# Kernel optimization log

Hardware: AMD Instinct MI355X
Metric: run time of the kernel (lower is better)

## Reference

```python
import jax, jax.numpy as jnp
import numpy as np

SXY_BF, SC_BF = 70.0, 12.0
COMPAT_BF, COMPAT_SPATIAL = 4.0, 2.0
SXY_SPATIAL = 6
NUM_ITER = 5
N_OUT = 21


def _gkern_depthwise(std, chans):
    # matches gkern(): sig_sq even -> r = sig_sq - 1, s = 2r+1
    sig_sq = std ** 2
    r = sig_sq if sig_sq % 2 else sig_sq - 1
    s = 2 * r + 1
    yy, xx = np.meshgrid(np.arange(s), np.arange(s), indexing='ij')
    k = np.exp(-(((yy - r) ** 2 + (xx - r) ** 2) / (2.0 * sig_sq)))
    k = k / k.sum()
    # original builds a [C,C,s,s] diagonal kernel == depthwise [C,1,s,s]
    return jnp.asarray(np.broadcast_to(k[None, None], (chans, 1, s, s)).copy(), jnp.float32)


def setup_inputs() -> dict:
    key = jax.random.key(0)
    k1, k2 = jax.random.split(key)
    unary = jax.random.uniform(k1, (2, N_OUT, 64, 64), dtype=jnp.float32)
    ref = jax.random.uniform(k2, (2, 3, 64, 64), dtype=jnp.float32) * 255.0  # RGB image
    gk = _gkern_depthwise(SXY_SPATIAL, N_OUT)
    kstd = jnp.asarray([SXY_BF, SXY_BF, SC_BF, SC_BF, SC_BF], jnp.float32)
    return {"unary": unary, "ref": ref, "gk": gk, "kstd": kstd}


def _crf_forward(unary, ref, gk, kstd):
    N, C, H, W = unary.shape
    P = H * W
    # stacked reference features: [y, x, r, g, b]
    yy, xx = jnp.meshgrid(jnp.arange(H, dtype=jnp.float32),
                          jnp.arange(W, dtype=jnp.float32), indexing='ij')
    grid = jnp.broadcast_to(jnp.stack([yy, xx])[None], (N, 2, H, W))
    stacked = jnp.concatenate([grid, ref], axis=1)  # [N,5,H,W]
    feats = (stacked / kstd[None, :, None, None]).reshape(N, -1, P).transpose(0, 2, 1)  # [N,P,5]
    # exact dense Gaussian (bilateral) kernel: K[p,q] = exp(-||f_p - f_q||^2 / 2)
    sq = jnp.sum(feats * feats, axis=-1)  # [N,P]
    d2 = sq[:, :, None] + sq[:, None, :] - 2.0 * jnp.einsum('npd,nqd->npq', feats, feats)
    K = jnp.exp(-0.5 * jnp.maximum(d2, 0.0))  # [N,P,P]

    U = jnp.log(jnp.clip(unary, 1e-5, 1.0))
    q = jax.nn.softmax(U, axis=1)
    pad = gk.shape[-1] // 2
    for i in range(NUM_ITER):
        qbf = jnp.einsum('npq,ncq->ncp', K, q.reshape(N, C, P)).reshape(N, C, H, W)
        qsf = jax.lax.conv_general_dilated(
            q, gk, window_strides=(1, 1), padding=[(pad, pad), (pad, pad)],
            feature_group_count=C, dimension_numbers=('NCHW', 'OIHW', 'NCHW'))
        q_hat = U + COMPAT_BF * qbf + COMPAT_SPATIAL * qsf
        q = jax.nn.softmax(q_hat, axis=1)  # normalize_final_iter=True
    return q


def reference(unary, ref, gk, kstd):
    return _crf_forward(unary, ref, gk, kstd)
```

## Files before the change

### kernel.cpp

```cpp
#include <hip/hip_runtime.h>
#include <math.h>

#ifndef __has_builtin
#define __has_builtin(x) 0
#endif
#if __has_builtin(__builtin_amdgcn_exp2f)
#define EXP2F(x) __builtin_amdgcn_exp2f(x)
#else
#define EXP2F(x) exp2f(x)
#endif

#define L2E  1.44269504088896340736f
#define RL2E 0.69314718055994530942f

#define NBATCH 2
#define NC 21
#define NP 4096
#define KR 35
#define KS 71

typedef _Float16 half_t;
typedef _Float16 h8 __attribute__((ext_vector_type(8)));
typedef _Float16 h4 __attribute__((ext_vector_type(4)));
typedef float f4 __attribute__((ext_vector_type(4)));
typedef float f2 __attribute__((ext_vector_type(2)));
#define MFMA16(a, b, c) __builtin_amdgcn_mfma_f32_16x16x32_f16((a), (b), (c), 0, 0, 0)

static __device__ __forceinline__ f2 pk_fma(f2 a, f2 b, f2 c) {
    f2 d;
    asm volatile("v_pk_fma_f32 %0, %1, %2, %3" : "=v"(d) : "v"(a), "v"(b), "v"(c));
    return d;
}
static __device__ __forceinline__ f2 pk_add(f2 a, f2 b) {
    f2 d;
    asm volatile("v_pk_add_f32 %0, %1, %2" : "=v"(d) : "v"(a), "v"(b));
    return d;
}

#define PTILE 128
#define NPT   32
#define SQ    16
#define CHUNK 256
#define STEPS 8
#define NBBIL (NBATCH * NPT * SQ)
#define NBCONV (NBATCH * NC)
#define SEGS_PER_S 1024
#define SEG_HALVES 256

#define OFF_QFEAT 0
#define OFF_QSOA  65536
#define OFF_UT    114688
#define OFF_QSF   311296
#define OFF_G     483328
#define OFF_QH16  485376
#define OFF_PART  845824

#define LDS_BYTES 27648
#define QLS_STRIDE 264

__global__ __launch_bounds__(256) void setup_kernel(
    const float* __restrict__ unary, const float* __restrict__ ref,
    const float* __restrict__ kstd, float* __restrict__ ws,
    float* __restrict__ outq)
{
    int gid = blockIdx.x * 256 + threadIdx.x;
    if (gid < 4096) {
        float s = 0.f;
        for (int t = -KR; t <= KR; ++t) s += expf(-(float)(t * t) * (1.0f / 72.0f));
        int y = gid >> 6, yp = gid & 63;
        int d = y - yp;
        float v = (d >= -KR && d <= KR) ? expf(-(float)(d * d) * (1.0f / 72.0f)) / s : 0.f;
        ((half_t*)(ws + OFF_G))[gid] = (half_t)v;
    }
    if (gid >= NBATCH * NP) return;
    int n = gid >> 12, p = gid & (NP - 1);
    int y = p >> 6, x = p & 63;
    float k0 = kstd[0], k1 = kstd[1], k2 = kstd[2], k3 = kstd[3], k4 = kstd[4];
    const float* rp = ref + n * 3 * NP + p;
    float f0 = (float)y / k0;
    float f1 = (float)x / k1;
    float f2_ = rp[0]      / k2;
    float f3 = rp[NP]     / k3;
    float f4_ = rp[2 * NP] / k4;
    float sq = f0*f0 + f1*f1 + f2_*f2_ + f3*f3 + f4_*f4_;
    float h  = -0.5f * L2E * sq;
    float* qf = ws + OFF_QFEAT + gid * 8;
    qf[0]=L2E*f0; qf[1]=L2E*f1; qf[2]=L2E*f2_; qf[3]=L2E*f3; qf[4]=L2E*f4_;
    qf[5]=h; qf[6]=0.f; qf[7]=0.f;
    float* qs = ws + OFF_QSOA;
    qs[0*8192 + gid] = L2E*f0;  qs[1*8192 + gid] = L2E*f1;
    qs[2*8192 + gid] = L2E*f2_; qs[3*8192 + gid] = L2E*f3;
    qs[4*8192 + gid] = L2E*f4_; qs[5*8192 + gid] = h;

    float U[NC], e[NC];
    const float* up = unary + n * NC * NP + p;
    float m = -1e30f;
    for (int c = 0; c < NC; ++c) {
        float u = up[c * NP];
        u = fminf(fmaxf(u, 1e-5f), 1.0f);
        U[c] = logf(u);
        m = fmaxf(m, U[c]);
    }
    float ssum = 0.f;
    for (int c = 0; c < NC; ++c) { e[c] = EXP2F(L2E * (U[c] - m)); ssum += e[c]; }
    float inv = 1.0f / ssum;
    float* ut = ws + OFF_UT + gid * 24;
    half_t* qh = (half_t*)(ws + OFF_QH16);
    for (int c = 0; c < NC; ++c) {
        float qv = e[c] * inv;
        ut[c] = U[c];
        qh[(n * 24 + c) * NP + p] = (half_t)qv;
        outq[(n * NC + c) * NP + p] = qv;
    }
    ut[21] = 0.f; ut[22] = 0.f; ut[23] = 0.f;
    qh[(n * 24 + 21) * NP + p] = (half_t)0.f;
    qh[(n * 24 + 22) * NP + p] = (half_t)0.f;
    qh[(n * 24 + 23) * NP + p] = (half_t)0.f;
}

__global__ __launch_bounds__(256) void bilat_conv_kernel(
    const float* __restrict__ qfeatA,
    const float* __restrict__ qsoa,
    const half_t* __restrict__ qh16,
    const half_t* __restrict__ gmat,
    half_t* __restrict__ part,
    float* __restrict__ qsf)
{
    __shared__ __align__(16) char lds[LDS_BYTES];
    int b = blockIdx.x;
    int tid = threadIdx.x;
    int l = tid & 63, w = tid >> 6;

    if (b < NBBIL) {
        int n  = b & 1;
        int pt = (b >> 1) & (NPT - 1);
        int s  = b >> 6;
        float*  qsoaS = (float*)lds;
        half_t* qls   = (half_t*)(lds + 6144);

        for (int i = tid; i < 6 * (CHUNK / 4); i += 256) {
            int d = i >> 6, g = i & 63;
            *(f4*)(qsoaS + d * CHUNK + g * 4) =
                *(const f4*)(qsoa + (size_t)d * 8192 + n * NP + s * CHUNK + g * 4);
        }
        for (int i = tid; i < 21 * (CHUNK / 8); i += 256) {
            int c = i >> 5, g = i & 31;
            *(h8*)(qls + c * QLS_STRIDE + g * 8) =
                *(const h8*)(qh16 + (size_t)(n * 24 + c) * NP + s * CHUNK + g * 8);
        }
        for (int i = tid; i < 11 * 33; i += 256) {
            int c = 21 + i / 33, g = i % 33;
            *(h8*)(qls + c * QLS_STRIDE + g * 8) = (h8)(half_t)0.f;
        }
        f2 pf2[2][5], ph2[2];
        #pragma unroll
        for (int mt = 0; mt < 2; ++mt) {
            const float* fp = qfeatA + (size_t)(n * NP + pt * PTILE + (w * 2 + mt) * 16 + (l & 15)) * 8;
            #pragma unroll
            for (int i = 0; i < 5; ++i) {
                float v = fp[i] * RL2E;
                pf2[mt][i] = (f2){v, v};
            }
            ph2[mt] = (f2){fp[5], fp[5]};
        }
        f4 acc[2][2];
        #pragma unroll
        for (int mt = 0; mt < 2; ++mt) { acc[mt][0] = (f4)0.f; acc[mt][1] = (f4)0.f; }
        int kq = (l >> 4) * 8;
        __syncthreads();

        for (int step = 0; step < STEPS; ++step) {
            int qbase = step * 32 + kq;
            h8 kv[2];
            #pragma unroll
            for (int hf = 0; hf < 2; ++hf) {
                f4 qf0 = *(const f4*)(qsoaS + 0 * CHUNK + qbase + hf * 4);
                f4 qf1 = *(const f4*)(qsoaS + 1 * CHUNK + qbase + hf * 4);
                f4 qf2 = *(const f4*)(qsoaS + 2 * CHUNK + qbase + hf * 4);
                f4 qf3 = *(const f4*)(qsoaS + 3 * CHUNK + qbase + hf * 4);
                f4 qf4 = *(const f4*)(qsoaS + 4 * CHUNK + qbase + hf * 4);
                f4 qf5 = *(const f4*)(qsoaS + 5 * CHUNK + qbase + hf * 4);
                #pragma unroll
                for (int pr = 0; pr < 2; ++pr) {
                    f2 q0 = {qf0[2*pr], qf0[2*pr+1]};
                    f2 q1 = {qf1[2*pr], qf1[2*pr+1]};
                    f2 q2 = {qf2[2*pr], qf2[2*pr+1]};
                    f2 q3 = {qf3[2*pr], qf3[2*pr+1]};
                    f2 q4 = {qf4[2*pr], qf4[2*pr+1]};
                    f2 qh2 = {qf5[2*pr], qf5[2*pr+1]};
                    #pragma unroll
                    for (int mt = 0; mt < 2; ++mt) {
                        f2 e = pk_add(qh2, ph2[mt]);
                        e = pk_fma(pf2[mt][0], q0, e);
                        e = pk_fma(pf2[mt][1], q1, e);
                        e = pk_fma(pf2[mt][2], q2, e);
                        e = pk_fma(pf2[mt][3], q3, e);
                        e = pk_fma(pf2[mt][4], q4, e);
                        kv[mt][hf * 4 + pr * 2]     = (half_t)EXP2F(e[0]);
                        kv[mt][hf * 4 + pr * 2 + 1] = (half_t)EXP2F(e[1]);
                    }
                }
            }
            h8 bf0 = *(const h8*)(qls + (size_t)(l & 15) * QLS_STRIDE + qbase);
            h8 bf1 = *(const h8*)(qls + (size_t)(16 + (l & 15)) * QLS_STRIDE + qbase);
            #pragma unroll
            for (int mt = 0; mt < 2; ++mt) {
                acc[mt][0] = MFMA16(kv[mt], bf0, acc[mt][0]);
                acc[mt][1] = MFMA16(kv[mt], bf1, acc[mt][1]);
            }
        }
        #pragma unroll
        for (int mt = 0; mt < 2; ++mt) {
            #pragma unroll
            for (int cht = 0; cht < 2; ++cht) {
                int segFlat = ((((s * 2 + n) * NPT + pt) * 4 + w) * 2 + mt) * 2 + cht;
                h4 hv;
                hv[0] = (half_t)acc[mt][cht][0];
                hv[1] = (half_t)acc[mt][cht][1];
                hv[2] = (half_t)acc[mt][cht][2];
                hv[3] = (half_t)acc[mt][cht][3];
                *(h4*)(part + (size_t)segFlat * SEG_HALVES + l * 4) = hv;
            }
        }
    } else {
        int cb = b - NBBIL;
        int n = cb / NC, c = cb % NC;
        half_t* qt = (half_t*)lds;
        half_t* gl = (half_t*)(lds + 9216);
        half_t* dl = (half_t*)(lds + 18432);

        for (int i = tid; i < 512; i += 256) {
            int row = i >> 3, g = i & 7;
            *(h8*)(gl + row * 72 + g * 8) = *(const h8*)(gmat + row * 64 + g * 8);
        }
        const half_t* qsrc = qh16 + (size_t)(n * 24 + c) * NP;
        for (int i = tid; i < 512; i += 256) {
            int row = i >> 3, g = i & 7;
            h8 v = *(const h8*)(qsrc + row * 64 + g * 8);
            #pragma unroll
            for (int k = 0; k < 8; ++k) qt[(g * 8 + k) * 72 + row] = v[k];
        }
        __syncthreads();

        int m0 = w * 16;
        f4 acc1[4];
        #pragma unroll
        for (int nt = 0; nt < 4; ++nt) acc1[nt] = (f4)0.f;
        #pragma unroll
        for (int ks = 0; ks < 2; ++ks) {
            h8 af = *(const h8*)(gl + (size_t)(m0 + (l & 15)) * 72 + ks * 32 + (l >> 4) * 8);
            #pragma unroll
            for (int nt = 0; nt < 4; ++nt) {
                h8 bf = *(const h8*)(qt + (size_t)(nt * 16 + (l & 15)) * 72 + ks * 32 + (l >> 4) * 8);
                acc1[nt] = MFMA16(af, bf, acc1[nt]);
            }
        }
        #pragma unroll
        for (int nt = 0; nt < 4; ++nt)
            #pragma unroll
            for (int r = 0; r < 4; ++r)
                dl[(size_t)(m0 + (l >> 4) * 4 + r) * 72 + nt * 16 + (l & 15)] = (half_t)acc1[nt][r];
        __syncthreads();

        f4 acc2[4];
        #pragma unroll
        for (int nt = 0; nt < 4; ++nt) acc2[nt] = (f4)0.f;
        #pragma unroll
        for (int ks = 0; ks < 2; ++ks) {
            h8 af = *(const h8*)(dl + (size_t)(m0 + (l & 15)) * 72 + ks * 32 + (l >> 4) * 8);
            #pragma unroll
            for (int nt = 0; nt < 4; ++nt) {
                h8 bf = *(const h8*)(gl + (size_t)(nt * 16 + (l & 15)) * 72 + ks * 32 + (l >> 4) * 8);
                acc2[nt] = MFMA16(af, bf, acc2[nt]);
            }
        }
        float* dst = qsf + (size_t)(n * NC + c) * NP;
        #pragma unroll
        for (int nt = 0; nt < 4; ++nt)
            #pragma unroll
            for (int r = 0; r < 4; ++r)
                dst[(size_t)(m0 + (l >> 4) * 4 + r) * 64 + nt * 16 + (l & 15)] = acc2[nt][r];
    }
}

__global__ __launch_bounds__(256) void reduce_update_kernel(
    const half_t* __restrict__ part, const float* __restrict__ ut_,
    const float* __restrict__ qsf, float* __restrict__ outq,
    half_t* __restrict__ qh16)
{
    __shared__ float red[4096];
    int rb = blockIdx.x;
    int tid = threadIdx.x;
    int n = rb & 1, pt = rb >> 1;

    float acc[16];
    #pragma unroll
    for (int k = 0; k < 16; ++k) acc[k] = 0.f;
    for (int s = 0; s < SQ; ++s) {
        size_t base = (size_t)(((s * 2 + n) * NPT + pt) * 16) * SEG_HALVES;
        #pragma unroll
        for (int k = 0; k < 4; ++k) {
            h4 v = *(const h4*)(part + base + (size_t)(k * 256 + tid) * 4);
            acc[k*4+0] += (float)v[0]; acc[k*4+1] += (float)v[1];
            acc[k*4+2] += (float)v[2]; acc[k*4+3] += (float)v[3];
        }
    }
    #pragma unroll
    for (int k = 0; k < 4; ++k)
        *(f4*)(red + (k * 256 + tid) * 4) =
            (f4){acc[k*4+0], acc[k*4+1], acc[k*4+2], acc[k*4+3]};
    __syncthreads();

    if (tid < PTILE) {
        int pp = tid;
        int p = pt * PTILE + pp;
        int gid = n * NP + p;
        int mt_g = pp >> 4;
        int wv = mt_g >> 1, mtl = mt_g & 1;
        int mrow = pp & 15;
        int lg = mrow >> 2, reg = mrow & 3;
        int segL = wv * 4 + mtl * 2;

        float lg_[NC], e[NC];
        const float* ut = ut_ + (size_t)gid * 24;
        const float* qs = qsf + (size_t)n * NC * NP + p;
        float m = -1e30f;
        #pragma unroll
        for (int c = 0; c < NC; ++c) {
            int cht = c >> 4, chL = c & 15;
            float qb = red[(segL + cht) * 256 + (lg * 16 + chL) * 4 + reg];
            float li = ut[c] + 4.0f * qb + 2.0f * qs[c * NP];
            lg_[c] = li;
            m = fmaxf(m, li);
        }
        float ssum = 0.f;
        #pragma unroll
        for (int c = 0; c < NC; ++c) { e[c] = EXP2F(L2E * (lg_[c] - m)); ssum += e[c]; }
        float inv = 1.0f / ssum;
        #pragma unroll
        for (int c = 0; c < NC; ++c) {
            float qv = e[c] * inv;
            outq[(size_t)(n * NC + c) * NP + p] = qv;
            qh16[(size_t)(n * 24 + c) * NP + p] = (half_t)qv;
        }
    }
}

extern "C" void kernel_launch(void* const* d_in, const int* in_sizes, int n_in,
                              void* d_out, int out_size, void* d_ws, size_t ws_size,
                              hipStream_t stream)
{
    const float* unary = (const float*)d_in[0];
    const float* ref   = (const float*)d_in[1];
    const float* kstd  = (const float*)d_in[3];
    float* ws   = (float*)d_ws;
    float* outq = (float*)d_out;

    const float*  qfeatA = ws + OFF_QFEAT;
    const float*  qsoa   = ws + OFF_QSOA;
    float*        ut     = ws + OFF_UT;
    float*        qsf    = ws + OFF_QSF;
    const half_t* gmat   = (const half_t*)(ws + OFF_G);
    half_t*       qh16   = (half_t*)(ws + OFF_QH16);
    half_t*       part   = (half_t*)(ws + OFF_PART);

    setup_kernel<<<32, 256, 0, stream>>>(unary, ref, kstd, ws, outq);
    for (int it = 0; it < 5; ++it) {
        bilat_conv_kernel<<<NBBIL + NBCONV, 256, 0, stream>>>(
            qfeatA, qsoa, qh16, gmat, part, qsf);
        reduce_update_kernel<<<64, 256, 0, stream>>>(part, ut, qsf, outq, qh16);
    }
}
```

Baseline: 155.0 us.

## Fuse setup and all CRF iterations into one cooperative persistent kernel

Replaces the eleven separate launches (setup, then bilateral/conv and reduce/update per iteration) with a single cooperative kernel. It uses grid-wide syncs between phases and keeps the query-feature chunk in LDS across iterations. Per-launch overhead and pipeline drain between tiny kernels should go away. The costs are the grid.sync barriers, a grid capped at 1024 co-resident blocks, and conv blocks doubling as bilateral blocks, which serialises work that used to run on extra blocks. The old multi-kernel path remains as a fallback when cooperative launch is unavailable.

```diff
diff --git a/kernel.cpp b/kernel.cpp
--- a/kernel.cpp
+++ b/kernel.cpp
@@ -1,5 +1,8 @@
 #include <hip/hip_runtime.h>
+#include <hip/hip_cooperative_groups.h>
 #include <math.h>
+
+namespace cg = cooperative_groups;
 
 #ifndef __has_builtin
 #define __has_builtin(x) 0
@@ -17,7 +20,7 @@
 #define NC 21
 #define NP 4096
 #define KR 35
-#define KS 71
+#define NUM_ITER 5
 
 typedef _Float16 half_t;
 typedef _Float16 h8 __attribute__((ext_vector_type(8)));
@@ -44,7 +47,6 @@
 #define STEPS 8
 #define NBBIL (NBATCH * NPT * SQ)
 #define NBCONV (NBATCH * NC)
-#define SEGS_PER_S 1024
 #define SEG_HALVES 256
 
 #define OFF_QFEAT 0
@@ -55,8 +57,293 @@
 #define OFF_QH16  485376
 #define OFF_PART  845824
 
-#define LDS_BYTES 27648
 #define QLS_STRIDE 264
+
+__global__ __launch_bounds__(256, 4) void crf_fused(
+    const float* __restrict__ unary, const float* __restrict__ ref,
+    const float* __restrict__ kstd, float* __restrict__ ws,
+    float* __restrict__ outq)
+{
+    __shared__ __align__(16) char lds[33792];
+    cg::grid_group grid = cg::this_grid();
+    const int b = blockIdx.x;
+    const int tid = threadIdx.x;
+    const int l = tid & 63, w = tid >> 6;
+
+    float*  qfeatA = ws + OFF_QFEAT;
+    float*  qsoa   = ws + OFF_QSOA;
+    float*  utb    = ws + OFF_UT;
+    float*  qsf    = ws + OFF_QSF;
+    half_t* gmat   = (half_t*)(ws + OFF_G);
+    half_t* qh16   = (half_t*)(ws + OFF_QH16);
+    half_t* part   = (half_t*)(ws + OFF_PART);
+
+    {
+        int gid = b * 256 + tid;
+        if (gid < 4096) {
+            float gs = 0.f;
+            for (int t = -KR; t <= KR; ++t) gs += expf(-(float)(t * t) * (1.0f / 72.0f));
+            int y = gid >> 6, yp = gid & 63;
+            int d = y - yp;
+            float v = (d >= -KR && d <= KR) ? expf(-(float)(d * d) * (1.0f / 72.0f)) / gs : 0.f;
+            gmat[gid] = (half_t)v;
+        }
+        if (gid < NBATCH * NP) {
+            int n = gid >> 12, p = gid & (NP - 1);
+            int y = p >> 6, x = p & 63;
+            float k0 = kstd[0], k1 = kstd[1], k2 = kstd[2], k3 = kstd[3], k4 = kstd[4];
+            const float* rp = ref + n * 3 * NP + p;
+            float f0 = (float)y / k0;
+            float f1 = (float)x / k1;
+            float f2_ = rp[0]      / k2;
+            float f3 = rp[NP]     / k3;
+            float f4_ = rp[2 * NP] / k4;
+            float sq = f0*f0 + f1*f1 + f2_*f2_ + f3*f3 + f4_*f4_;
+            float h  = -0.5f * L2E * sq;
+            float* qf = qfeatA + gid * 8;
+            qf[0]=L2E*f0; qf[1]=L2E*f1; qf[2]=L2E*f2_; qf[3]=L2E*f3; qf[4]=L2E*f4_;
+            qf[5]=h; qf[6]=0.f; qf[7]=0.f;
+            qsoa[0*8192 + gid] = L2E*f0;  qsoa[1*8192 + gid] = L2E*f1;
+            qsoa[2*8192 + gid] = L2E*f2_; qsoa[3*8192 + gid] = L2E*f3;
+            qsoa[4*8192 + gid] = L2E*f4_; qsoa[5*8192 + gid] = h;
+
+            float U[NC], eU[NC];
+            const float* up = unary + n * NC * NP + p;
+            float m = -1e30f;
+            for (int c = 0; c < NC; ++c) {
+                float u = up[c * NP];
+                u = fminf(fmaxf(u, 1e-5f), 1.0f);
+                U[c] = logf(u);
+                m = fmaxf(m, U[c]);
+            }
+            float ssum = 0.f;
+            for (int c = 0; c < NC; ++c) { eU[c] = EXP2F(L2E * (U[c] - m)); ssum += eU[c]; }
+            float inv = 1.0f / ssum;
+            float* utp = utb + gid * 24;
+            for (int c = 0; c < NC; ++c) {
+                utp[c] = U[c];
+                qh16[(n * 24 + c) * NP + p] = (half_t)(eU[c] * inv);
+            }
+            utp[21] = 0.f; utp[22] = 0.f; utp[23] = 0.f;
+            qh16[(n * 24 + 21) * NP + p] = (half_t)0.f;
+            qh16[(n * 24 + 22) * NP + p] = (half_t)0.f;
+            qh16[(n * 24 + 23) * NP + p] = (half_t)0.f;
+        }
+    }
+    grid.sync();
+
+    const int nB  = b & 1;
+    const int ptB = (b >> 1) & (NPT - 1);
+    const int sB  = b >> 6;
+
+    {
+        float* qsoaS = (float*)lds;
+        for (int i = tid; i < 6 * (CHUNK / 4); i += 256) {
+            int d = i >> 6, g = i & 63;
+            *(f4*)(qsoaS + d * CHUNK + g * 4) =
+                *(const f4*)(qsoa + (size_t)d * 8192 + nB * NP + sB * CHUNK + g * 4);
+        }
+    }
+
+    for (int it = 0; it < NUM_ITER; ++it) {
+        {
+            float*  qsoaS = (float*)lds;
+            half_t* qls   = (half_t*)(lds + 6144);
+
+            for (int i = tid; i < 21 * (CHUNK / 8); i += 256) {
+                int c = i >> 5, g = i & 31;
+                *(h8*)(qls + c * QLS_STRIDE + g * 8) =
+                    *(const h8*)(qh16 + (size_t)(nB * 24 + c) * NP + sB * CHUNK + g * 8);
+            }
+            if (it == 0 || b < NBCONV) {
+                for (int i = tid; i < 11 * 33; i += 256) {
+                    int c = 21 + i / 33, g = i % 33;
+                    *(h8*)(qls + c * QLS_STRIDE + g * 8) = (h8)(half_t)0.f;
+                }
+            }
+            f2 pf2[2][5], ph2[2];
+            #pragma unroll
+            for (int mt = 0; mt < 2; ++mt) {
+                const float* fp = qfeatA + (size_t)(nB * NP + ptB * PTILE + (w * 2 + mt) * 16 + (l & 15)) * 8;
+                #pragma unroll
+                for (int i = 0; i < 5; ++i) {
+                    float v = fp[i] * RL2E;
+                    pf2[mt][i] = (f2){v, v};
+                }
+                ph2[mt] = (f2){fp[5], fp[5]};
+            }
+            f4 acc[2][2];
+            #pragma unroll
+            for (int mt = 0; mt < 2; ++mt) { acc[mt][0] = (f4)0.f; acc[mt][1] = (f4)0.f; }
+            int kq = (l >> 4) * 8;
+            __syncthreads();
+
+            for (int step = 0; step < STEPS; ++step) {
+                int qbase = step * 32 + kq;
+                h8 kv[2];
+                #pragma unroll
+                for (int hf = 0; hf < 2; ++hf) {
+                    f4 qf0 = *(const f4*)(qsoaS + 0 * CHUNK + qbase + hf * 4);
+                    f4 qf1 = *(const f4*)(qsoaS + 1 * CHUNK + qbase + hf * 4);
+                    f4 qf2 = *(const f4*)(qsoaS + 2 * CHUNK + qbase + hf * 4);
+                    f4 qf3 = *(const f4*)(qsoaS + 3 * CHUNK + qbase + hf * 4);
+                    f4 qf4 = *(const f4*)(qsoaS + 4 * CHUNK + qbase + hf * 4);
+                    f4 qf5 = *(const f4*)(qsoaS + 5 * CHUNK + qbase + hf * 4);
+                    #pragma unroll
+                    for (int pr = 0; pr < 2; ++pr) {
+                        f2 q0 = {qf0[2*pr], qf0[2*pr+1]};
+                        f2 q1 = {qf1[2*pr], qf1[2*pr+1]};
+                        f2 q2 = {qf2[2*pr], qf2[2*pr+1]};
+                        f2 q3 = {qf3[2*pr], qf3[2*pr+1]};
+                        f2 q4 = {qf4[2*pr], qf4[2*pr+1]};
+                        f2 qh2 = {qf5[2*pr], qf5[2*pr+1]};
+                        #pragma unroll
+                        for (int mt = 0; mt < 2; ++mt) {
+                            f2 e = pk_add(qh2, ph2[mt]);
+                            e = pk_fma(pf2[mt][0], q0, e);
+                            e = pk_fma(pf2[mt][1], q1, e);
+                            e = pk_fma(pf2[mt][2], q2, e);
+                            e = pk_fma(pf2[mt][3], q3, e);
+                            e = pk_fma(pf2[mt][4], q4, e);
+                            kv[mt][hf * 4 + pr * 2]     = (half_t)EXP2F(e[0]);
+                            kv[mt][hf * 4 + pr * 2 + 1] = (half_t)EXP2F(e[1]);
+                        }
+                    }
+                }
+                h8 bf0 = *(const h8*)(qls + (size_t)(l & 15) * QLS_STRIDE + qbase);
+                h8 bf1 = *(const h8*)(qls + (size_t)(16 + (l & 15)) * QLS_STRIDE + qbase);
+                #pragma unroll
+                for (int mt = 0; mt < 2; ++mt) {
+                    acc[mt][0] = MFMA16(kv[mt], bf0, acc[mt][0]);
+                    acc[mt][1] = MFMA16(kv[mt], bf1, acc[mt][1]);
+                }
+            }
+            #pragma unroll
+            for (int mt = 0; mt < 2; ++mt) {
+                #pragma unroll
+                for (int cht = 0; cht < 2; ++cht) {
+                    int segFlat = ((((sB * 2 + nB) * NPT + ptB) * 4 + w) * 2 + mt) * 2 + cht;
+                    h4 hv;
+                    hv[0] = (half_t)acc[mt][cht][0];
+                    hv[1] = (half_t)acc[mt][cht][1];
+                    hv[2] = (half_t)acc[mt][cht][2];
+                    hv[3] = (half_t)acc[mt][cht][3];
+                    *(h4*)(part + (size_t)segFlat * SEG_HALVES + l * 4) = hv;
+                }
+            }
+        }
+
+        if (b < NBCONV) {
+            __syncthreads();
+            int n2 = b / NC, c2 = b % NC;
+            half_t* qt = (half_t*)(lds + 6144);
+            half_t* gl = (half_t*)(lds + 15360);
+            half_t* dl = (half_t*)(lds + 24576);
+
+            for (int i = tid; i < 512; i += 256) {
+                int row = i >> 3, g = i & 7;
+                *(h8*)(gl + row * 72 + g * 8) = *(const h8*)(gmat + row * 64 + g * 8);
+            }
+            const half_t* qsrc = qh16 + (size_t)(n2 * 24 + c2) * NP;
+            for (int i = tid; i < 512; i += 256) {
+                int row = i >> 3, g = i & 7;
+                h8 v = *(const h8*)(qsrc + row * 64 + g * 8);
+                #pragma unroll
+                for (int k = 0; k < 8; ++k) qt[(g * 8 + k) * 72 + row] = v[k];
+            }
+            __syncthreads();
+
+            int m0 = w * 16;
+            f4 acc1[4];
+            #pragma unroll
+            for (int nt = 0; nt < 4; ++nt) acc1[nt] = (f4)0.f;
+            #pragma unroll
+            for (int ks = 0; ks < 2; ++ks) {
+                h8 af = *(const h8*)(gl + (size_t)(m0 + (l & 15)) * 72 + ks * 32 + (l >> 4) * 8);
+                #pragma unroll
+                for (int nt = 0; nt < 4; ++nt) {
+                    h8 bf = *(const h8*)(qt + (size_t)(nt * 16 + (l & 15)) * 72 + ks * 32 + (l >> 4) * 8);
+                    acc1[nt] = MFMA16(af, bf, acc1[nt]);
+                }
+            }
+            #pragma unroll
+            for (int nt = 0; nt < 4; ++nt)
+                #pragma unroll
+                for (int r = 0; r < 4; ++r)
+                    dl[(size_t)(m0 + (l >> 4) * 4 + r) * 72 + nt * 16 + (l & 15)] = (half_t)acc1[nt][r];
+            __syncthreads();
+
+            f4 acc2[4];
+            #pragma unroll
+            for (int nt = 0; nt < 4; ++nt) acc2[nt] = (f4)0.f;
+            #pragma unroll
+            for (int ks = 0; ks < 2; ++ks) {
+                h8 af = *(const h8*)(dl + (size_t)(m0 + (l & 15)) * 72 + ks * 32 + (l >> 4) * 8);
+                #pragma unroll
+                for (int nt = 0; nt < 4; ++nt) {
+                    h8 bf = *(const h8*)(gl + (size_t)(nt * 16 + (l & 15)) * 72 + ks * 32 + (l >> 4) * 8);
+                    acc2[nt] = MFMA16(af, bf, acc2[nt]);
+                }
+            }
+            float* dst = qsf + (size_t)(n2 * NC + c2) * NP;
+            #pragma unroll
+            for (int nt = 0; nt < 4; ++nt)
+                #pragma unroll
+                for (int r = 0; r < 4; ++r)
+                    dst[(size_t)(m0 + (l >> 4) * 4 + r) * 64 + nt * 16 + (l & 15)] = acc2[nt][r];
+        }
+        grid.sync();
+
+        if (b < 256) {
+            int n = b & 1, pt = (b >> 1) & 31, wq = b >> 6;
+            float* red = (float*)(lds + 6144);
+            int lseg = w;
+            float a0 = 0.f, a1 = 0.f, a2 = 0.f, a3 = 0.f;
+            for (int s = 0; s < SQ; ++s) {
+                size_t segF = (size_t)((((s * 2 + n) * NPT + pt) * 4 + wq) * 4 + lseg);
+                h4 v = *(const h4*)(part + segF * SEG_HALVES + (size_t)l * 4);
+                a0 += (float)v[0]; a1 += (float)v[1]; a2 += (float)v[2]; a3 += (float)v[3];
+            }
+            *(f4*)(red + tid * 4) = (f4){a0, a1, a2, a3};
+            __syncthreads();
+
+            if (tid < 32) {
+                int pp = tid;
+                int p = pt * PTILE + wq * 32 + pp;
+                int gid = n * NP + p;
+                int mtl = pp >> 4, mrow = pp & 15;
+                int lg2 = mrow >> 2, reg = mrow & 3;
+
+                const float* ut = utb + (size_t)gid * 24;
+                const float* qs = qsf + (size_t)n * NC * NP + p;
+                float e[NC];
+                float m = -1e30f;
+                #pragma unroll
+                for (int c = 0; c < NC; ++c) {
+                    int cht = c >> 4, chL = c & 15;
+                    float qb = red[(mtl * 2 + cht) * 256 + (lg2 * 16 + chL) * 4 + reg];
+                    float li = ut[c] + 4.0f * qb + 2.0f * qs[c * NP];
+                    e[c] = li;
+                    m = fmaxf(m, li);
+                }
+                float ssum = 0.f;
+                #pragma unroll
+                for (int c = 0; c < NC; ++c) { float v = EXP2F(L2E * (e[c] - m)); e[c] = v; ssum += v; }
+                float inv = 1.0f / ssum;
+                if (it == NUM_ITER - 1) {
+                    #pragma unroll
+                    for (int c = 0; c < NC; ++c)
+                        outq[(size_t)(n * NC + c) * NP + p] = e[c] * inv;
+                } else {
+                    #pragma unroll
+                    for (int c = 0; c < NC; ++c)
+                        qh16[(size_t)(n * 24 + c) * NP + p] = (half_t)(e[c] * inv);
+                }
+            }
+        }
+        if (it < NUM_ITER - 1) grid.sync();
+    }
+}
 
 __global__ __launch_bounds__(256) void setup_kernel(
     const float* __restrict__ unary, const float* __restrict__ ref,
@@ -119,14 +406,11 @@
 }
 
 __global__ __launch_bounds__(256) void bilat_conv_kernel(
-    const float* __restrict__ qfeatA,
-    const float* __restrict__ qsoa,
-    const half_t* __restrict__ qh16,
-    const half_t* __restrict__ gmat,
-    half_t* __restrict__ part,
-    float* __restrict__ qsf)
+    const float* __restrict__ qfeatA, const float* __restrict__ qsoa,
+    const half_t* __restrict__ qh16, const half_t* __restrict__ gmat,
+    half_t* __restrict__ part, float* __restrict__ qsf)
 {
-    __shared__ __align__(16) char lds[LDS_BYTES];
+    __shared__ __align__(16) char lds[27648];
     int b = blockIdx.x;
     int tid = threadIdx.x;
     int l = tid & 63, w = tid >> 6;
@@ -356,18 +640,38 @@
     float* ws   = (float*)d_ws;
     float* outq = (float*)d_out;
 
-    const float*  qfeatA = ws + OFF_QFEAT;
-    const float*  qsoa   = ws + OFF_QSOA;
-    float*        ut     = ws + OFF_UT;
-    float*        qsf    = ws + OFF_QSF;
-    const half_t* gmat   = (const half_t*)(ws + OFF_G);
-    half_t*       qh16   = (half_t*)(ws + OFF_QH16);
-    half_t*       part   = (half_t*)(ws + OFF_PART);
-
-    setup_kernel<<<32, 256, 0, stream>>>(unary, ref, kstd, ws, outq);
-    for (int it = 0; it < 5; ++it) {
-        bilat_conv_kernel<<<NBBIL + NBCONV, 256, 0, stream>>>(
-            qfeatA, qsoa, qh16, gmat, part, qsf);
-        reduce_update_kernel<<<64, 256, 0, stream>>>(part, ut, qsf, outq, qh16);
+    static int coop_ok = -1;
+    if (coop_ok < 0) {
+        int dev = 0, has = 0, nb = 0, ncu = 0;
+        (void)hipGetDevice(&dev);
+        (void)hipDeviceGetAttribute(&has, hipDeviceAttributeCooperativeLaunch, dev);
+        (void)hipDeviceGetAttribute(&ncu, hipDeviceAttributeMultiprocessorCount, dev);
+        (void)hipOccupancyMaxActiveBlocksPerMultiprocessor(&nb, crf_fused, 256, 0);
+        coop_ok = (has && (long)nb * ncu >= NBBIL) ? 1 : 0;
+    }
+
+    int launched = 0;
+    if (coop_ok) {
+        void* kargs[] = {(void*)&unary, (void*)&ref, (void*)&kstd, (void*)&ws, (void*)&outq};
+        hipError_t err = hipLaunchCooperativeKernel(crf_fused, dim3(NBBIL), dim3(256),
+                                                    kargs, 0u, stream);
+        if (err == hipSuccess) launched = 1;
+        else { (void)hipGetLastError(); coop_ok = 0; }
+    }
+    if (!launched) {
+        const float*  qfeatA = ws + OFF_QFEAT;
+        const float*  qsoa   = ws + OFF_QSOA;
+        float*        ut     = ws + OFF_UT;
+        float*        qsf    = ws + OFF_QSF;
+        const half_t* gmat   = (const half_t*)(ws + OFF_G);
+        half_t*       qh16   = (half_t*)(ws + OFF_QH16);
+        half_t*       part   = (half_t*)(ws + OFF_PART);
+
+        setup_kernel<<<32, 256, 0, stream>>>(unary, ref, kstd, ws, outq);
+        for (int it = 0; it < NUM_ITER; ++it) {
+            bilat_conv_kernel<<<NBBIL + NBCONV, 256, 0, stream>>>(
+                qfeatA, qsoa, qh16, gmat, part, qsf);
+            reduce_update_kernel<<<64, 256, 0, stream>>>(part, ut, qsf, outq, qh16);
+        }
     }
 }
```

After: 155.0 us. Within noise of the previous version (+0.1%).

## Cache bilateral kernel matrix in fp16 on first iteration and widen reduce grid

Applied to the files above, without the earlier changes.

On the first iteration the bilateral kernel writes each computed exp(-d²/2) fp16 tile to a workspace buffer. Later iterations read those tiles back instead of recomputing the pairwise features and exponentials, which moves the cost from exp and FMA ALU work to roughly 64 MB of memory traffic per iteration. The reduce/softmax kernel is split across 4x more blocks, each handling 32 pixels, and it writes fp32 output only on the last iteration and fp16 q only on the others. The cached matrix lives within one call, so nothing is reused across calls.

```diff
diff --git a/kernel.cpp b/kernel.cpp
--- a/kernel.cpp
+++ b/kernel.cpp
@@ -17,7 +17,7 @@
 #define NC 21
 #define NP 4096
 #define KR 35
-#define KS 71
+#define NUM_ITER 5
 
 typedef _Float16 half_t;
 typedef _Float16 h8 __attribute__((ext_vector_type(8)));
@@ -44,7 +44,6 @@
 #define STEPS 8
 #define NBBIL (NBATCH * NPT * SQ)
 #define NBCONV (NBATCH * NC)
-#define SEGS_PER_S 1024
 #define SEG_HALVES 256
 
 #define OFF_QFEAT 0
@@ -54,6 +53,7 @@
 #define OFF_G     483328
 #define OFF_QH16  485376
 #define OFF_PART  845824
+#define OFF_KMAT  2942976
 
 #define LDS_BYTES 27648
 #define QLS_STRIDE 264
@@ -124,7 +124,9 @@
     const half_t* __restrict__ qh16,
     const half_t* __restrict__ gmat,
     half_t* __restrict__ part,
-    float* __restrict__ qsf)
+    float* __restrict__ qsf,
+    half_t* __restrict__ kmat,
+    int first)
 {
     __shared__ __align__(16) char lds[LDS_BYTES];
     int b = blockIdx.x;
@@ -138,10 +140,12 @@
         float*  qsoaS = (float*)lds;
         half_t* qls   = (half_t*)(lds + 6144);
 
-        for (int i = tid; i < 6 * (CHUNK / 4); i += 256) {
-            int d = i >> 6, g = i & 63;
-            *(f4*)(qsoaS + d * CHUNK + g * 4) =
-                *(const f4*)(qsoa + (size_t)d * 8192 + n * NP + s * CHUNK + g * 4);
+        if (first) {
+            for (int i = tid; i < 6 * (CHUNK / 4); i += 256) {
+                int d = i >> 6, g = i & 63;
+                *(f4*)(qsoaS + d * CHUNK + g * 4) =
+                    *(const f4*)(qsoa + (size_t)d * 8192 + n * NP + s * CHUNK + g * 4);
+            }
         }
         for (int i = tid; i < 21 * (CHUNK / 8); i += 256) {
             int c = i >> 5, g = i & 31;
@@ -152,61 +156,83 @@
             int c = 21 + i / 33, g = i % 33;
             *(h8*)(qls + c * QLS_STRIDE + g * 8) = (h8)(half_t)0.f;
         }
-        f2 pf2[2][5], ph2[2];
-        #pragma unroll
-        for (int mt = 0; mt < 2; ++mt) {
-            const float* fp = qfeatA + (size_t)(n * NP + pt * PTILE + (w * 2 + mt) * 16 + (l & 15)) * 8;
-            #pragma unroll
-            for (int i = 0; i < 5; ++i) {
-                float v = fp[i] * RL2E;
-                pf2[mt][i] = (f2){v, v};
-            }
-            ph2[mt] = (f2){fp[5], fp[5]};
-        }
+        half_t* kbase = kmat + (size_t)((b * 4 + w) * 2) * 8 * 512 + (size_t)l * 8;
+
         f4 acc[2][2];
         #pragma unroll
         for (int mt = 0; mt < 2; ++mt) { acc[mt][0] = (f4)0.f; acc[mt][1] = (f4)0.f; }
         int kq = (l >> 4) * 8;
-        __syncthreads();
-
-        for (int step = 0; step < STEPS; ++step) {
-            int qbase = step * 32 + kq;
-            h8 kv[2];
-            #pragma unroll
-            for (int hf = 0; hf < 2; ++hf) {
-                f4 qf0 = *(const f4*)(qsoaS + 0 * CHUNK + qbase + hf * 4);
-                f4 qf1 = *(const f4*)(qsoaS + 1 * CHUNK + qbase + hf * 4);
-                f4 qf2 = *(const f4*)(qsoaS + 2 * CHUNK + qbase + hf * 4);
-                f4 qf3 = *(const f4*)(qsoaS + 3 * CHUNK + qbase + hf * 4);
-                f4 qf4 = *(const f4*)(qsoaS + 4 * CHUNK + qbase + hf * 4);
-                f4 qf5 = *(const f4*)(qsoaS + 5 * CHUNK + qbase + hf * 4);
+
+        if (first) {
+            f2 pf2[2][5], ph2[2];
+            #pragma unroll
+            for (int mt = 0; mt < 2; ++mt) {
+                const float* fp = qfeatA + (size_t)(n * NP + pt * PTILE + (w * 2 + mt) * 16 + (l & 15)) * 8;
                 #pragma unroll
-                for (int pr = 0; pr < 2; ++pr) {
-                    f2 q0 = {qf0[2*pr], qf0[2*pr+1]};
-                    f2 q1 = {qf1[2*pr], qf1[2*pr+1]};
-                    f2 q2 = {qf2[2*pr], qf2[2*pr+1]};
-                    f2 q3 = {qf3[2*pr], qf3[2*pr+1]};
-                    f2 q4 = {qf4[2*pr], qf4[2*pr+1]};
-                    f2 qh2 = {qf5[2*pr], qf5[2*pr+1]};
+                for (int i = 0; i < 5; ++i) {
+                    float v = fp[i] * RL2E;
+                    pf2[mt][i] = (f2){v, v};
+                }
+                ph2[mt] = (f2){fp[5], fp[5]};
+            }
+            __syncthreads();
+
+            for (int step = 0; step < STEPS; ++step) {
+                int qbase = step * 32 + kq;
+                h8 kv[2];
+                #pragma unroll
+                for (int hf = 0; hf < 2; ++hf) {
+                    f4 qf0 = *(const f4*)(qsoaS + 0 * CHUNK + qbase + hf * 4);
+                    f4 qf1 = *(const f4*)(qsoaS + 1 * CHUNK + qbase + hf * 4);
+                    f4 qf2 = *(const f4*)(qsoaS + 2 * CHUNK + qbase + hf * 4);
+                    f4 qf3 = *(const f4*)(qsoaS + 3 * CHUNK + qbase + hf * 4);
+                    f4 qf4 = *(const f4*)(qsoaS + 4 * CHUNK + qbase + hf * 4);
+                    f4 qf5 = *(const f4*)(qsoaS + 5 * CHUNK + qbase + hf * 4);
                     #pragma unroll
-                    for (int mt = 0; mt < 2; ++mt) {
-                        f2 e = pk_add(qh2, ph2[mt]);
-                        e = pk_fma(pf2[mt][0], q0, e);
-                        e = pk_fma(pf2[mt][1], q1, e);
-                        e = pk_fma(pf2[mt][2], q2, e);
-                        e = pk_fma(pf2[mt][3], q3, e);
-                        e = pk_fma(pf2[mt][4], q4, e);
-                        kv[mt][hf * 4 + pr * 2]     = (half_t)EXP2F(e[0]);
-                        kv[mt][hf * 4 + pr * 2 + 1] = (half_t)EXP2F(e[1]);
+                    for (int pr = 0; pr < 2; ++pr) {
+                        f2 q0 = {qf0[2*pr], qf0[2*pr+1]};
+                        f2 q1 = {qf1[2*pr], qf1[2*pr+1]};
+                        f2 q2 = {qf2[2*pr], qf2[2*pr+1]};
+                        f2 q3 = {qf3[2*pr], qf3[2*pr+1]};
+                        f2 q4 = {qf4[2*pr], qf4[2*pr+1]};
+                        f2 qh2 = {qf5[2*pr], qf5[2*pr+1]};
+                        #pragma unroll
+                        for (int mt = 0; mt < 2; ++mt) {
+                            f2 e = pk_add(qh2, ph2[mt]);
+                            e = pk_fma(pf2[mt][0], q0, e);
+                            e = pk_fma(pf2[mt][1], q1, e);
+                            e = pk_fma(pf2[mt][2], q2, e);
+                            e = pk_fma(pf2[mt][3], q3, e);
+                            e = pk_fma(pf2[mt][4], q4, e);
+                            kv[mt][hf * 4 + pr * 2]     = (half_t)EXP2F(e[0]);
+                            kv[mt][hf * 4 + pr * 2 + 1] = (half_t)EXP2F(e[1]);
+                        }
                     }
                 }
-            }
-            h8 bf0 = *(const h8*)(qls + (size_t)(l & 15) * QLS_STRIDE + qbase);
-            h8 bf1 = *(const h8*)(qls + (size_t)(16 + (l & 15)) * QLS_STRIDE + qbase);
-            #pragma unroll
-            for (int mt = 0; mt < 2; ++mt) {
-                acc[mt][0] = MFMA16(kv[mt], bf0, acc[mt][0]);
-                acc[mt][1] = MFMA16(kv[mt], bf1, acc[mt][1]);
+                *(h8*)(kbase + (size_t)(0 * 8 + step) * 512) = kv[0];
+                *(h8*)(kbase + (size_t)(1 * 8 + step) * 512) = kv[1];
+
+                h8 bf0 = *(const h8*)(qls + (size_t)(l & 15) * QLS_STRIDE + qbase);
+                h8 bf1 = *(const h8*)(qls + (size_t)(16 + (l & 15)) * QLS_STRIDE + qbase);
+                #pragma unroll
+                for (int mt = 0; mt < 2; ++mt) {
+                    acc[mt][0] = MFMA16(kv[mt], bf0, acc[mt][0]);
+                    acc[mt][1] = MFMA16(kv[mt], bf1, acc[mt][1]);
+                }
+            }
+        } else {
+            __syncthreads();
+            #pragma unroll
+            for (int step = 0; step < STEPS; ++step) {
+                int qbase = step * 32 + kq;
+                h8 kv0 = *(const h8*)(kbase + (size_t)(0 * 8 + step) * 512);
+                h8 kv1 = *(const h8*)(kbase + (size_t)(1 * 8 + step) * 512);
+                h8 bf0 = *(const h8*)(qls + (size_t)(l & 15) * QLS_STRIDE + qbase);
+                h8 bf1 = *(const h8*)(qls + (size_t)(16 + (l & 15)) * QLS_STRIDE + qbase);
+                acc[0][0] = MFMA16(kv0, bf0, acc[0][0]);
+                acc[0][1] = MFMA16(kv0, bf1, acc[0][1]);
+                acc[1][0] = MFMA16(kv1, bf0, acc[1][0]);
+                acc[1][1] = MFMA16(kv1, bf1, acc[1][1]);
             }
         }
         #pragma unroll
@@ -286,62 +312,54 @@
 __global__ __launch_bounds__(256) void reduce_update_kernel(
     const half_t* __restrict__ part, const float* __restrict__ ut_,
     const float* __restrict__ qsf, float* __restrict__ outq,
-    half_t* __restrict__ qh16)
+    half_t* __restrict__ qh16, int last)
 {
-    __shared__ float red[4096];
+    __shared__ float red[1024];
     int rb = blockIdx.x;
     int tid = threadIdx.x;
-    int n = rb & 1, pt = rb >> 1;
-
-    float acc[16];
-    #pragma unroll
-    for (int k = 0; k < 16; ++k) acc[k] = 0.f;
+    int n = rb & 1, pt = (rb >> 1) & 31, wq = rb >> 6;
+    int lseg = tid >> 6, l = tid & 63;
+
+    float a0 = 0.f, a1 = 0.f, a2 = 0.f, a3 = 0.f;
     for (int s = 0; s < SQ; ++s) {
-        size_t base = (size_t)(((s * 2 + n) * NPT + pt) * 16) * SEG_HALVES;
-        #pragma unroll
-        for (int k = 0; k < 4; ++k) {
-            h4 v = *(const h4*)(part + base + (size_t)(k * 256 + tid) * 4);
-            acc[k*4+0] += (float)v[0]; acc[k*4+1] += (float)v[1];
-            acc[k*4+2] += (float)v[2]; acc[k*4+3] += (float)v[3];
-        }
-    }
-    #pragma unroll
-    for (int k = 0; k < 4; ++k)
-        *(f4*)(red + (k * 256 + tid) * 4) =
-            (f4){acc[k*4+0], acc[k*4+1], acc[k*4+2], acc[k*4+3]};
+        size_t segF = (size_t)((((s * 2 + n) * NPT + pt) * 4 + wq) * 4 + lseg);
+        h4 v = *(const h4*)(part + segF * SEG_HALVES + (size_t)l * 4);
+        a0 += (float)v[0]; a1 += (float)v[1]; a2 += (float)v[2]; a3 += (float)v[3];
+    }
+    *(f4*)(red + tid * 4) = (f4){a0, a1, a2, a3};
     __syncthreads();
 
-    if (tid < PTILE) {
+    if (tid < 32) {
         int pp = tid;
-        int p = pt * PTILE + pp;
+        int p = pt * PTILE + wq * 32 + pp;
         int gid = n * NP + p;
-        int mt_g = pp >> 4;
-        int wv = mt_g >> 1, mtl = mt_g & 1;
-        int mrow = pp & 15;
-        int lg = mrow >> 2, reg = mrow & 3;
-        int segL = wv * 4 + mtl * 2;
-
-        float lg_[NC], e[NC];
+        int mtl = pp >> 4, mrow = pp & 15;
+        int lg2 = mrow >> 2, reg = mrow & 3;
+
         const float* ut = ut_ + (size_t)gid * 24;
         const float* qs = qsf + (size_t)n * NC * NP + p;
+        float e[NC];
         float m = -1e30f;
         #pragma unroll
         for (int c = 0; c < NC; ++c) {
             int cht = c >> 4, chL = c & 15;
-            float qb = red[(segL + cht) * 256 + (lg * 16 + chL) * 4 + reg];
+            float qb = red[(mtl * 2 + cht) * 256 + (lg2 * 16 + chL) * 4 + reg];
             float li = ut[c] + 4.0f * qb + 2.0f * qs[c * NP];
-            lg_[c] = li;
+            e[c] = li;
             m = fmaxf(m, li);
         }
         float ssum = 0.f;
         #pragma unroll
-        for (int c = 0; c < NC; ++c) { e[c] = EXP2F(L2E * (lg_[c] - m)); ssum += e[c]; }
+        for (int c = 0; c < NC; ++c) { float v = EXP2F(L2E * (e[c] - m)); e[c] = v; ssum += v; }
         float inv = 1.0f / ssum;
-        #pragma unroll
-        for (int c = 0; c < NC; ++c) {
-            float qv = e[c] * inv;
-            outq[(size_t)(n * NC + c) * NP + p] = qv;
-            qh16[(size_t)(n * 24 + c) * NP + p] = (half_t)qv;
+        if (last) {
+            #pragma unroll
+            for (int c = 0; c < NC; ++c)
+                outq[(size_t)(n * NC + c) * NP + p] = e[c] * inv;
+        } else {
+            #pragma unroll
+            for (int c = 0; c < NC; ++c)
+                qh16[(size_t)(n * 24 + c) * NP + p] = (half_t)(e[c] * inv);
         }
     }
 }
@@ -363,11 +381,13 @@
     const half_t* gmat   = (const half_t*)(ws + OFF_G);
     half_t*       qh16   = (half_t*)(ws + OFF_QH16);
     half_t*       part   = (half_t*)(ws + OFF_PART);
+    half_t*       kmat   = (half_t*)(ws + OFF_KMAT);
 
     setup_kernel<<<32, 256, 0, stream>>>(unary, ref, kstd, ws, outq);
-    for (int it = 0; it < 5; ++it) {
+    for (int it = 0; it < NUM_ITER; ++it) {
         bilat_conv_kernel<<<NBBIL + NBCONV, 256, 0, stream>>>(
-            qfeatA, qsoa, qh16, gmat, part, qsf);
-        reduce_update_kernel<<<64, 256, 0, stream>>>(part, ut, qsf, outq, qh16);
-    }
-}
+            qfeatA, qsoa, qh16, gmat, part, qsf, kmat, it == 0 ? 1 : 0);
+        reduce_update_kernel<<<256, 256, 0, stream>>>(
+            part, ut, qsf, outq, qh16, it == NUM_ITER - 1 ? 1 : 0);
+    }
+}
```

Measured after the change: 159.2 us. +2.7%, slower.
